# Optimization experiments

Hardware: AMD Instinct MI355X
Metric: run time of the kernel (lower is better)

## Reference

```python
import jax, jax.numpy as jnp
import numpy as np

DIM = 64
NUM_FEAT = 14
NUM_OUT = 105
N_NODES = 8192
N_EDGES = 16384
N_GRAPHS = 256
N_STEMS = 2048
N_JBONDS = 1024


def lrelu(v):
    return jax.nn.leaky_relu(v, 0.01)


def setup_inputs() -> dict:
    key = jax.random.key(0)
    ks = jax.random.split(key, 40)
    def rn(k, shape, s=0.1):
        return jax.random.normal(k, shape, dtype=jnp.float32) * s
    inp = {}
    inp['x'] = jax.random.normal(ks[0], (N_NODES, NUM_FEAT), dtype=jnp.float32)
    inp['edge_attr'] = jax.random.uniform(ks[1], (N_EDGES, 4), dtype=jnp.float32)
    inp['edge_index'] = jax.random.randint(ks[2], (2, N_EDGES), 0, N_NODES)
    inp['batch'] = jnp.sort(jax.random.randint(ks[3], (N_NODES,), 0, N_GRAPHS))
    inp['stem_atmidx'] = jax.random.randint(ks[4], (N_STEMS,), 0, N_NODES)
    inp['jbond_atmidx'] = jax.random.randint(ks[5], (N_JBONDS, 2), 0, N_NODES)
    # lin0
    inp['lin0_w'] = rn(ks[6], (NUM_FEAT, DIM)); inp['lin0_b'] = rn(ks[7], (DIM,))
    # NNConv edge net: Linear(4,dim) -> LeakyReLU -> Linear(dim, dim*dim)
    inp['net_w1'] = rn(ks[8], (4, DIM)); inp['net_b1'] = rn(ks[9], (DIM,))
    inp['net_w2'] = rn(ks[10], (DIM, DIM * DIM), 0.02); inp['net_b2'] = rn(ks[11], (DIM * DIM,), 0.02)
    # NNConv root weight + bias
    inp['conv_root'] = rn(ks[12], (DIM, DIM)); inp['conv_bias'] = rn(ks[13], (DIM,))
    # GRU (torch gate order r,z,n); stored [in, 3*dim]
    inp['gru_w_ih'] = rn(ks[14], (DIM, 3 * DIM)); inp['gru_w_hh'] = rn(ks[15], (DIM, 3 * DIM))
    inp['gru_b_ih'] = rn(ks[16], (3 * DIM,)); inp['gru_b_hh'] = rn(ks[17], (3 * DIM,))
    # node2stem MLP
    inp['n2s_w1'] = rn(ks[18], (DIM, DIM)); inp['n2s_b1'] = rn(ks[19], (DIM,))
    inp['n2s_w2'] = rn(ks[20], (DIM, NUM_OUT)); inp['n2s_b2'] = rn(ks[21], (NUM_OUT,))
    # node2jbond MLP
    inp['n2j_w1'] = rn(ks[22], (DIM, DIM)); inp['n2j_b1'] = rn(ks[23], (DIM,))
    inp['n2j_w2'] = rn(ks[24], (DIM, 1)); inp['n2j_b2'] = rn(ks[25], (1,))
    # Set2Set LSTM(2*dim -> dim), torch gate order i,f,g,o; stored [in, 4*dim]
    inp['s2s_w_ih'] = rn(ks[26], (2 * DIM, 4 * DIM)); inp['s2s_w_hh'] = rn(ks[27], (DIM, 4 * DIM))
    inp['s2s_b_ih'] = rn(ks[28], (4 * DIM,)); inp['s2s_b_hh'] = rn(ks[29], (4 * DIM,))
    # lin_out
    inp['lin_out_w'] = rn(ks[30], (2 * DIM, 2)); inp['lin_out_b'] = rn(ks[31], (2,))
    return inp


def reference(x, edge_attr, lin0_w, lin0_b, net_w1, net_b1, net_w2, net_b2,
              conv_root, conv_bias, gru_w_ih, gru_w_hh, gru_b_ih, gru_b_hh,
              n2s_w1, n2s_b1, n2s_w2, n2s_b2, n2j_w1, n2j_b1, n2j_w2, n2j_b2,
              s2s_w_ih, s2s_w_hh, s2s_b_ih, s2s_b_hh, lin_out_w, lin_out_b,
              edge_index, batch, stem_atmidx, jbond_atmidx):
    N = x.shape[0]
    src, dst = edge_index[0], edge_index[1]
    out = lrelu(x @ lin0_w + lin0_b)          # [N, dim]
    h = out
    # edge-conditioned weights (edge_attr is constant across the 6 iterations)
    ew = (lrelu(edge_attr @ net_w1 + net_b1) @ net_w2 + net_b2).reshape(-1, DIM, DIM)  # [E,dim,dim]
    deg = jnp.maximum(jax.ops.segment_sum(jnp.ones_like(dst, dtype=x.dtype), dst, num_segments=N), 1.0)[:, None]
    for _ in range(6):
        msg = jnp.einsum('ei,eio->eo', out[src], ew)                        # per-edge matmul
        agg = jax.ops.segment_sum(msg, dst, num_segments=N) / deg          # scatter-mean
        m = lrelu(agg + out @ conv_root + conv_bias)
        # GRU update (torch gate order r,z,n)
        gi = m @ gru_w_ih + gru_b_ih
        gh = h @ gru_w_hh + gru_b_hh
        ir, iz, inn = jnp.split(gi, 3, axis=-1)
        hr, hz, hn = jnp.split(gh, 3, axis=-1)
        r = jax.nn.sigmoid(ir + hr)
        z = jax.nn.sigmoid(iz + hz)
        n = jnp.tanh(inn + r * hn)
        h = (1.0 - z) * n + z * h
        out = h
    # per-stem block logits
    stem_preds = lrelu(out[stem_atmidx] @ n2s_w1 + n2s_b1) @ n2s_w2 + n2s_b2  # [S, num_out]
    # jbond: gather both endpoints, predict scalar, mean over the pair
    jb = out[jbond_atmidx.reshape(-1)]
    jpred = lrelu(jb @ n2j_w1 + n2j_b1) @ n2j_w2 + n2j_b2                     # [2J,1]
    jbond_preds = jpred.reshape(jbond_atmidx.shape).mean(axis=1)              # [J]
    # Set2Set, processing_steps=1
    B = N_GRAPHS
    hS = jnp.zeros((B, DIM), x.dtype)
    cS = jnp.zeros((B, DIM), x.dtype)
    q_star = jnp.zeros((B, 2 * DIM), x.dtype)
    gates = q_star @ s2s_w_ih + s2s_b_ih + hS @ s2s_w_hh + s2s_b_hh
    gi_, gf_, gg_, go_ = jnp.split(gates, 4, axis=-1)
    cS = jax.nn.sigmoid(gf_) * cS + jax.nn.sigmoid(gi_) * jnp.tanh(gg_)
    hS = jax.nn.sigmoid(go_) * jnp.tanh(cS)
    q = hS                                                                    # [B, dim]
    e = jnp.sum(out * q[batch], axis=-1)                                      # [N]
    emax = jax.ops.segment_max(e, batch, num_segments=B)
    a_un = jnp.exp(e - emax[batch])
    a = a_un / jax.ops.segment_sum(a_un, batch, num_segments=B)[batch]
    r_pool = jax.ops.segment_sum(a[:, None] * out, batch, num_segments=B)     # [B, dim]
    q_star = jnp.concatenate([q, r_pool], axis=1)                             # [B, 2*dim]
    scalar_outs = q_star @ lin_out_w + lin_out_b                              # [B, 2]
    return (scalar_outs, stem_preds, jbond_preds)
```

## Files before the change

### kernel.cpp

```cpp
#include <hip/hip_runtime.h>

#define DIM 64
#define NF 14
#define NOUT 105
#define NN 8192
#define NE 16384
#define NB 256
#define NS 2048
#define NJ 1024
#define KTOT 4160

#define C_X      0
#define C_EA     114688
#define C_L0W    180224
#define C_L0B    181120
#define C_NW1    181184
#define C_NB1    181440
#define C_NW2    181504
#define C_NB2    443648
#define C_CRT    447744
#define C_CB     451840
#define C_GWIH   451904
#define C_GWHH   464192
#define C_GBIH   476480
#define C_GBHH   476672
#define C_SW1    476864
#define C_SB1    480960
#define C_SW2    481024
#define C_SB2    487744
#define C_JW1    487856
#define C_JB1    491952
#define C_JW2    492016
#define C_JB2    492080
#define C_S2IH   492088
#define C_S2HH   492344
#define C_LOW    492600
#define C_LOB    492856
#define C_TOT    492864

typedef float f32x4 __attribute__((ext_vector_type(4)));
typedef short bf16x8 __attribute__((ext_vector_type(8)));

__device__ __forceinline__ float bf2f(unsigned short u){
  union { unsigned int i; float f; } v; v.i = ((unsigned int)u) << 16; return v.f;
}
__device__ __forceinline__ unsigned short f2bf(float f){
  union { float f; unsigned int i; } v; v.f = f;
  unsigned int x = v.i;
  return (unsigned short)((x + 0x7FFFu + ((x >> 16) & 1u)) >> 16);
}
__device__ __forceinline__ float sigm(float x){ return 1.f / (1.f + __expf(-x)); }
__device__ __forceinline__ float tanh_f(float x){
  x = fminf(10.f, fmaxf(-10.f, x));
  float e = __expf(2.f * x);
  return (e - 1.f) / (e + 1.f);
}
__device__ __forceinline__ float lrelu(float x){ return x > 0.f ? x : 0.01f * x; }

__device__ __forceinline__ float wred_sum(float v){
  #pragma unroll
  for (int off = 32; off > 0; off >>= 1) v += __shfl_xor(v, off, 64);
  return v;
}
__device__ __forceinline__ float wred_max(float v){
  #pragma unroll
  for (int off = 32; off > 0; off >>= 1) v = fmaxf(v, __shfl_xor(v, off, 64));
  return v;
}


__global__ void k_detect(const unsigned short* __restrict__ ea, int* __restrict__ flag){
  __shared__ int cnt;
  if (threadIdx.x == 0) cnt = 0;
  __syncthreads();
  int c = 0;
  for (int i = threadIdx.x; i < 8192; i += 256) c += (ea[2*i] >> 15) & 1;
  atomicAdd(&cnt, c);
  __syncthreads();
  if (threadIdx.x == 0) *flag = (cnt > 100) ? 1 : 0;
}

struct CvtArgs {
  const void* src[26];
  int n[26];
  int off[26];
};

__global__ void k_cvt(CvtArgs a, const int* __restrict__ flag, unsigned short* __restrict__ dst){
  bool f32 = (*flag != 0);
  int gid = blockIdx.x * blockDim.x + threadIdx.x, gs = gridDim.x * blockDim.x;
  #pragma unroll 1
  for (int j = 0; j < 26; ++j){
    const void* s = a.src[j];
    int n = a.n[j], o = a.off[j];
    for (int i = gid; i < n; i += gs)
      dst[o + i] = f32 ? f2bf(((const float*)s)[i]) : ((const unsigned short*)s)[i];
  }
}


__global__ void k_deg(const int* __restrict__ ei, float* __restrict__ deg){
  int e = blockIdx.x * blockDim.x + threadIdx.x;
  if (e < NE) atomicAdd(&deg[ei[NE + e]], 1.0f);
}

__global__ __launch_bounds__(256) void k_scan(const float* __restrict__ deg,
                                              int* __restrict__ offsets, int* __restrict__ cursor){
  __shared__ int part[256];
  int t = threadIdx.x;
  int s = 0;
  #pragma unroll 4
  for (int i = 0; i < 32; ++i) s += (int)deg[t*32 + i];
  part[t] = s;
  __syncthreads();
  for (int d = 1; d < 256; d <<= 1){
    int v = (t >= d) ? part[t - d] : 0;
    __syncthreads();
    part[t] += v;
    __syncthreads();
  }
  int run = (t == 0) ? 0 : part[t - 1];
  #pragma unroll 4
  for (int i = 0; i < 32; ++i){
    int n = t*32 + i;
    offsets[n] = run;
    cursor[n] = 0;
    run += (int)deg[n];
  }
  if (t == 255) offsets[NN] = run;
}

__global__ void k_fill(const int* __restrict__ ei, const int* __restrict__ offsets,
                       int* __restrict__ cursor, int* __restrict__ list){
  int e = blockIdx.x * blockDim.x + threadIdx.x;
  if (e < NE){
    int dst = ei[NE + e];
    int pos = atomicAdd(&cursor[dst], 1);
    list[offsets[dst] + pos] = e;
  }
}

__global__ void k_lin0(const unsigned short* __restrict__ cvt,
                       float* __restrict__ actF, unsigned short* __restrict__ actB){
  const unsigned short* x = cvt + C_X;
  const unsigned short* w = cvt + C_L0W;
  const unsigned short* b = cvt + C_L0B;
  int idx = blockIdx.x * blockDim.x + threadIdx.x;
  int n = idx >> 6, d = idx & 63;
  float acc = bf2f(b[d]);
  #pragma unroll
  for (int f = 0; f < NF; ++f) acc += bf2f(x[n*NF + f]) * bf2f(w[f*DIM + d]);
  float v = lrelu(acc);
  actF[idx] = v; actB[idx] = f2bf(v);
}

__global__ void k_u(const unsigned short* __restrict__ cvt, unsigned short* __restrict__ u){
  const unsigned short* ea = cvt + C_EA;
  const unsigned short* w  = cvt + C_NW1;
  const unsigned short* b  = cvt + C_NB1;
  int idx = blockIdx.x * blockDim.x + threadIdx.x;
  int e = idx >> 6, d = idx & 63;
  float acc = bf2f(b[d]);
  #pragma unroll
  for (int f = 0; f < 4; ++f) acc += bf2f(ea[e*4 + f]) * bf2f(w[f*DIM + d]);
  u[idx] = f2bf(lrelu(acc));
}

__global__ void k_w2t(const unsigned short* __restrict__ cvt, unsigned short* __restrict__ w2t){
  const unsigned short* w2 = cvt + C_NW2;
  int t = blockIdx.x * blockDim.x + threadIdx.x;
  int n = t >> 6, k = t & 63;
  w2t[t] = w2[k*4096 + (n & 63)*64 + (n >> 6)];
}

__global__ void k_w2r(const unsigned short* __restrict__ cvt, unsigned short* __restrict__ w2rt){
  const unsigned short* w2 = cvt + C_NW2;
  const unsigned short* b2 = cvt + C_NB2;
  int t = blockIdx.x * blockDim.x + threadIdx.x;
  int o = t / KTOT, k = t - o * KTOT;
  unsigned short v = (k < 4096) ? w2[(k >> 6) * 4096 + (k & 63) * 64 + o]
                                : b2[(k - 4096) * 64 + o];
  w2rt[t] = v;
}

__global__ void k_prep(const unsigned short* __restrict__ cvt,
                       unsigned short* __restrict__ crt, unsigned short* __restrict__ btg,
                       float* __restrict__ cbg, float* __restrict__ qv){
  const unsigned short* cr  = cvt + C_CRT;
  const unsigned short* wih = cvt + C_GWIH;
  const unsigned short* whh = cvt + C_GWHH;
  const unsigned short* bih = cvt + C_GBIH;
  const unsigned short* bhh = cvt + C_GBHH;
  const unsigned short* s2sbih = cvt + C_S2IH;
  const unsigned short* s2sbhh = cvt + C_S2HH;
  int tid = threadIdx.x;
  for (int t = tid; t < 4096; t += 256){ int n = t & 63, k = t >> 6; crt[n*64 + k] = cr[k*64 + n]; }
  for (int t = tid; t < 32768; t += 256){
    int nidx = t >> 7, kidx = t & 127;
    int g = nidx >> 6, d = nidx & 63, ki = kidx & 63;
    unsigned short v = 0;
    if (kidx < 64){
      if (g == 0) v = wih[ki*192 + d];
      else if (g == 1) v = wih[ki*192 + 64 + d];
      else if (g == 2) v = wih[ki*192 + 128 + d];
    } else {
      if (g == 0) v = whh[ki*192 + d];
      else if (g == 1) v = whh[ki*192 + 64 + d];
      else if (g == 3) v = whh[ki*192 + 128 + d];
    }
    btg[nidx*128 + kidx] = v;
  }
  if (tid < 256){
    int g = tid >> 6, d = tid & 63;
    float v;
    if (g == 0) v = bf2f(bih[d]) + bf2f(bhh[d]);
    else if (g == 1) v = bf2f(bih[64 + d]) + bf2f(bhh[64 + d]);
    else if (g == 2) v = bf2f(bih[128 + d]);
    else v = bf2f(bhh[128 + d]);
    cbg[tid] = v;
  }
  if (tid < 64){
    float gi = bf2f(s2sbih[tid])       + bf2f(s2sbhh[tid]);
    float gg = bf2f(s2sbih[128 + tid]) + bf2f(s2sbhh[128 + tid]);
    float go = bf2f(s2sbih[192 + tid]) + bf2f(s2sbhh[192 + tid]);
    float c = sigm(gi) * tanh_f(gg);
    qv[tid] = sigm(go) * tanh_f(c);
  }
}


__global__ __launch_bounds__(256) void k_ew(const unsigned short* __restrict__ z,
                                            const unsigned short* __restrict__ w2t,
                                            const unsigned short* __restrict__ cvt,
                                            unsigned short* __restrict__ ew){
  const unsigned short* b2 = cvt + C_NB2;
  __shared__ __align__(16) unsigned short tile[4][4096];
  int w = threadIdx.x >> 6, lane = threadIdx.x & 63;
  int lm = lane & 15, q8 = (lane >> 4) * 8, rq = (lane >> 4) * 4;
  int e0 = blockIdx.x * 64;
  int n0 = blockIdx.y * 256 + w * 64;
  f32x4 acc[4][4];
  #pragma unroll
  for (int mt = 0; mt < 4; ++mt)
    #pragma unroll
    for (int nt = 0; nt < 4; ++nt) acc[mt][nt] = (f32x4){0.f, 0.f, 0.f, 0.f};
  #pragma unroll
  for (int kk = 0; kk < 2; ++kk){
    bf16x8 af[4], bfr[4];
    #pragma unroll
    for (int mt = 0; mt < 4; ++mt)
      af[mt] = *(const bf16x8*)&z[(size_t)(e0 + mt*16 + lm)*64 + kk*32 + q8];
    #pragma unroll
    for (int nt = 0; nt < 4; ++nt)
      bfr[nt] = *(const bf16x8*)&w2t[(size_t)(n0 + nt*16 + lm)*64 + kk*32 + q8];
    #pragma unroll
    for (int mt = 0; mt < 4; ++mt)
      #pragma unroll
      for (int nt = 0; nt < 4; ++nt)
        acc[mt][nt] = __builtin_amdgcn_mfma_f32_16x16x32_bf16(af[mt], bfr[nt], acc[mt][nt], 0, 0, 0);
  }
  #pragma unroll
  for (int nt = 0; nt < 4; ++nt){
    int col = nt*16 + lm;
    int gcol = n0 + col;
    float bb = bf2f(b2[((gcol & 63) << 6) | (gcol >> 6)]);
    #pragma unroll
    for (int mt = 0; mt < 4; ++mt)
      #pragma unroll
      for (int r = 0; r < 4; ++r){
        int row = mt*16 + rq + r;
        int phys = (col >> 3) ^ (row & 7);
        tile[w][row*64 + phys*8 + (col & 7)] = f2bf(acc[mt][nt][r] + bb);
      }
  }
  #pragma unroll
  for (int it = 0; it < 8; ++it){
    int row = it*8 + (lane >> 3);
    int c16 = lane & 7;
    int phys = c16 ^ (row & 7);
    bf16x8 v = *(const bf16x8*)&tile[w][row*64 + phys*8];
    *(bf16x8*)&ew[(size_t)(e0 + row)*4096 + n0 + c16*8] = v;
  }
}

__global__ __launch_bounds__(256) void k_msgv(const unsigned short* __restrict__ actB,
                                              const unsigned short* __restrict__ ew,
                                              const int* __restrict__ ei,
                                              unsigned short* __restrict__ msgv){
  __shared__ __align__(16) float sact[4][64];
  int w = threadIdx.x >> 6, lane = threadIdx.x & 63;
  int e = blockIdx.x * 4 + w;
  int src = ei[e];
  sact[w][lane] = bf2f(actB[(size_t)src*64 + lane]);
  __syncthreads();
  const unsigned short* ep = ew + (size_t)e*4096 + (size_t)lane*64;
  float acc = 0.f;
  #pragma unroll
  for (int t = 0; t < 8; ++t){
    bf16x8 v = *(const bf16x8*)(ep + t*8);
    f32x4 sa = *(const f32x4*)&sact[w][t*8];
    f32x4 sb = *(const f32x4*)&sact[w][t*8 + 4];
    acc += bf2f((unsigned short)v[0]) * sa[0];
    acc += bf2f((unsigned short)v[1]) * sa[1];
    acc += bf2f((unsigned short)v[2]) * sa[2];
    acc += bf2f((unsigned short)v[3]) * sa[3];
    acc += bf2f((unsigned short)v[4]) * sb[0];
    acc += bf2f((unsigned short)v[5]) * sb[1];
    acc += bf2f((unsigned short)v[6]) * sb[2];
    acc += bf2f((unsigned short)v[7]) * sb[3];
  }
  msgv[(size_t)e*64 + lane] = f2bf(acc);
}

__global__ __launch_bounds__(256) void k_agg(const unsigned short* __restrict__ msgv,
                                             const int* __restrict__ offsets,
                                             const int* __restrict__ list,
                                             float* __restrict__ agg){
  int w = threadIdx.x >> 6, lane = threadIdx.x & 63;
  int v = blockIdx.x * 4 + w;
  int ib = offsets[v], ie = offsets[v + 1];
  float acc = 0.f;
  for (int j = ib; j < ie; ++j){
    int e = list[j];
    acc += bf2f(msgv[(size_t)e*64 + lane]);
  }
  agg[(size_t)v*64 + lane] = acc;
}


__global__ __launch_bounds__(256) void k_msgf(const unsigned short* __restrict__ actB,
                                              const unsigned short* __restrict__ z,
                                              const unsigned short* __restrict__ w2rt,
                                              const int* __restrict__ ei,
                                              float* __restrict__ agg){
  __shared__ __align__(16) unsigned short sz[256 * 8];
  int w = threadIdx.x >> 6, lane = threadIdx.x & 63;
  int lm = lane & 15, q8 = (lane >> 4) * 8, rq = (lane >> 4) * 4;
  int e0 = blockIdx.x * 256;
  int s  = blockIdx.y;
  {
    int t = threadIdx.x;
    *(uint4*)&sz[t * 8] = *(const uint4*)&z[(size_t)(e0 + t) * 64 + s * 8];
  }
  __syncthreads();
  uint4 apack[4][2];
  #pragma unroll
  for (int mt = 0; mt < 4; ++mt){
    int src = ei[e0 + w*64 + mt*16 + lm];
    apack[mt][0] = *(const uint4*)&actB[(size_t)src * 64 + q8];
    apack[mt][1] = *(const uint4*)&actB[(size_t)src * 64 + 32 + q8];
  }
  f32x4 acc[4][4];
  #pragma unroll
  for (int mt = 0; mt < 4; ++mt)
    #pragma unroll
    for (int nt = 0; nt < 4; ++nt) acc[mt][nt] = (f32x4){0.f, 0.f, 0.f, 0.f};
  int kk0 = s * 16;
  int nk = (s == 7) ? 18 : 16;
  for (int c = 0; c < nk; ++c){
    int kk = kk0 + c;
    bf16x8 bfr[4];
    #pragma unroll
    for (int nt = 0; nt < 4; ++nt)
      bfr[nt] = *(const bf16x8*)&w2rt[(size_t)(nt*16 + lm) * KTOT + kk*32 + q8];
    #pragma unroll
    for (int mt = 0; mt < 4; ++mt){
      float zf = 1.0f;
      if (kk < 128){
        int erow = w*64 + mt*16 + lm;
        zf = bf2f(sz[erow * 8 + ((kk >> 1) & 7)]);
      }
      uint4 ap = apack[mt][kk & 1];
      bf16x8 af;
      #pragma unroll
      for (int h = 0; h < 4; ++h){
        unsigned int dw = ((const unsigned int*)&ap)[h];
        float flo = __uint_as_float(dw << 16) * zf;
        float fhi = __uint_as_float(dw & 0xFFFF0000u) * zf;
        unsigned int pk = ((unsigned int)f2bf(flo)) | (((unsigned int)f2bf(fhi)) << 16);
        ((unsigned int*)&af)[h] = pk;
      }
      #pragma unroll
      for (int nt = 0; nt < 4; ++nt)
        acc[mt][nt] = __builtin_amdgcn_mfma_f32_16x16x32_bf16(af, bfr[nt], acc[mt][nt], 0, 0, 0);
    }
  }
  #pragma unroll
  for (int mt = 0; mt < 4; ++mt){
    #pragma unroll
    for (int r = 0; r < 4; ++r){
      int dst = ei[NE + e0 + w*64 + mt*16 + rq + r];
      #pragma unroll
      for (int nt = 0; nt < 4; ++nt)
        atomicAdd(&agg[(size_t)dst * 64 + nt*16 + lm], acc[mt][nt][r]);
    }
  }
}


__global__ __launch_bounds__(256) void k_gru(const unsigned short* __restrict__ actB_in,
                                             const float* __restrict__ actF_in,
                                             const float* __restrict__ agg, const float* __restrict__ deg,
                                             const unsigned short* __restrict__ crt,
                                             const unsigned short* __restrict__ cvt,
                                             const unsigned short* __restrict__ btg,
                                             const float* __restrict__ cbg,
                                             float* __restrict__ actF_out, unsigned short* __restrict__ actB_out){
  const unsigned short* cbias = cvt + C_CB;
  __shared__ __align__(16) unsigned short s_frag[2*4*16*8];
  int w = threadIdx.x >> 6, lane = threadIdx.x & 63;
  int lm = lane & 15, q = lane >> 4;
  int q8 = q*8, rq = q*4;
  int r0 = blockIdx.x * 16;
  f32x4 am = (f32x4){0.f, 0.f, 0.f, 0.f};
  #pragma unroll
  for (int kk = 0; kk < 2; ++kk){
    bf16x8 a = *(const bf16x8*)&actB_in[(size_t)(r0 + lm)*64 + kk*32 + q8];
    bf16x8 b = *(const bf16x8*)&crt[(size_t)(w*16 + lm)*64 + kk*32 + q8];
    am = __builtin_amdgcn_mfma_f32_16x16x32_bf16(a, b, am, 0, 0, 0);
  }
  {
    int col = w*16 + lm;
    float cb = bf2f(cbias[col]);
    int kk2 = w >> 1, q2 = (w & 1)*2 + (lm >> 3), j = lm & 7;
    #pragma unroll
    for (int r = 0; r < 4; ++r){
      int row = r0 + rq + r;
      float dg = fmaxf(deg[row], 1.f);
      float v = am[r] + agg[(size_t)row*64 + col] / dg + cb;
      s_frag[((kk2*4 + q2)*16 + (rq + r))*8 + j] = f2bf(lrelu(v));
    }
  }
  __syncthreads();
  f32x4 g[4];
  #pragma unroll
  for (int t = 0; t < 4; ++t) g[t] = (f32x4){0.f, 0.f, 0.f, 0.f};
  #pragma unroll
  for (int kk = 0; kk < 4; ++kk){
    bf16x8 a;
    if (kk < 2) a = *(const bf16x8*)&s_frag[(kk*4 + q)*128 + lm*8];
    else        a = *(const bf16x8*)&actB_in[(size_t)(r0 + lm)*64 + (kk - 2)*32 + q8];
    #pragma unroll
    for (int t = 0; t < 4; ++t){
      bf16x8 b = *(const bf16x8*)&btg[(size_t)(t*64 + w*16 + lm)*128 + kk*32 + q8];
      g[t] = __builtin_amdgcn_mfma_f32_16x16x32_bf16(a, b, g[t], 0, 0, 0);
    }
  }
  {
    int d = w*16 + lm;
    float cb_r = cbg[d], cb_z = cbg[64 + d], cb_n = cbg[128 + d], cb_h = cbg[192 + d];
    #pragma unroll
    for (int r = 0; r < 4; ++r){
      int row = r0 + rq + r;
      float rr = sigm(g[0][r] + cb_r);
      float zz = sigm(g[1][r] + cb_z);
      float nn = tanh_f(g[2][r] + cb_n + rr * (g[3][r] + cb_h));
      float ho = actF_in[(size_t)row*64 + d];
      float hn2 = (1.f - zz) * nn + zz * ho;
      actF_out[(size_t)row*64 + d] = hn2;
      actB_out[(size_t)row*64 + d] = f2bf(hn2);
    }
  }
}


__device__ __forceinline__ int lower_bound_batch(const int* b, int val){
  int lo = 0, hi = NN;
  while (lo < hi){ int mid = (lo + hi) >> 1; if (b[mid] < val) lo = mid + 1; else hi = mid; }
  return lo;
}

__device__ __forceinline__ void store_out(void* outp, const int* flag, size_t idx, float v){
  if (*flag) ((float*)outp)[idx] = v;
  else       ((unsigned short*)outp)[idx] = f2bf(v);
}

__global__ __launch_bounds__(64) void k_graph(const float* __restrict__ act,
                                              const int* __restrict__ batch, const float* __restrict__ qv,
                                              const unsigned short* __restrict__ cvt,
                                              const int* __restrict__ flag,
                                              void* __restrict__ outp){
  const unsigned short* lw = cvt + C_LOW;
  const unsigned short* lb = cvt + C_LOB;
  __shared__ float se[512];
  int b = blockIdx.x, lane = threadIdx.x;
  int lo = lower_bound_batch(batch, b);
  int hi = lower_bound_batch(batch, b + 1);
  int cnt = hi - lo; if (cnt > 512) cnt = 512;
  float qvl = qv[lane];
  for (int ii = 0; ii < cnt; ++ii){
    float p = act[(size_t)(lo + ii)*64 + lane] * qvl;
    p = wred_sum(p);
    if (lane == 0) se[ii] = p;
  }
  __syncthreads();
  float em = -3.4e38f;
  for (int ii = lane; ii < cnt; ii += 64) em = fmaxf(em, se[ii]);
  em = wred_max(em);
  float sm = 0.f;
  for (int ii = lane; ii < cnt; ii += 64) sm += __expf(se[ii] - em);
  float denom = wred_sum(sm);
  float rp = 0.f;
  for (int ii = 0; ii < cnt; ++ii) rp += __expf(se[ii] - em) * act[(size_t)(lo + ii)*64 + lane];
  if (cnt > 0 && denom > 0.f) rp /= denom;
  float s0 = qvl*bf2f(lw[lane*2])     + rp*bf2f(lw[(64 + lane)*2]);
  float s1 = qvl*bf2f(lw[lane*2 + 1]) + rp*bf2f(lw[(64 + lane)*2 + 1]);
  s0 = wred_sum(s0); s1 = wred_sum(s1);
  if (lane == 0){
    store_out(outp, flag, b*2,     s0 + bf2f(lb[0]));
    store_out(outp, flag, b*2 + 1, s1 + bf2f(lb[1]));
  }
}

__global__ __launch_bounds__(256) void k_stem(const float* __restrict__ act, const int* __restrict__ sidx,
                                              const unsigned short* __restrict__ cvt,
                                              const int* __restrict__ flag,
                                              void* __restrict__ outp){
  const unsigned short* w1 = cvt + C_SW1;
  const unsigned short* b1 = cvt + C_SB1;
  const unsigned short* w2 = cvt + C_SW2;
  const unsigned short* b2 = cvt + C_SB2;
  __shared__ float sa[4][64], st[4][64];
  int w = threadIdx.x >> 6, lane = threadIdx.x & 63;
  int s = blockIdx.x * 4 + w;
  int a = sidx[s];
  sa[w][lane] = act[(size_t)a*64 + lane];
  __syncthreads();
  float t = bf2f(b1[lane]);
  #pragma unroll 8
  for (int i = 0; i < 64; ++i) t += sa[w][i] * bf2f(w1[i*64 + lane]);
  st[w][lane] = lrelu(t);
  __syncthreads();
  size_t base = 512 + (size_t)s * NOUT;
  float v = bf2f(b2[lane]);
  #pragma unroll 8
  for (int d = 0; d < 64; ++d) v += st[w][d] * bf2f(w2[d*NOUT + lane]);
  store_out(outp, flag, base + lane, v);
  int o2 = 64 + lane;
  if (o2 < NOUT){
    float v2 = bf2f(b2[o2]);
    #pragma unroll 8
    for (int d = 0; d < 64; ++d) v2 += st[w][d] * bf2f(w2[d*NOUT + o2]);
    store_out(outp, flag, base + o2, v2);
  }
}

__global__ __launch_bounds__(256) void k_jbond(const float* __restrict__ act, const int* __restrict__ jidx,
                                               const unsigned short* __restrict__ cvt,
                                               const int* __restrict__ flag,
                                               void* __restrict__ outp){
  const unsigned short* w1 = cvt + C_JW1;
  const unsigned short* b1 = cvt + C_JB1;
  const unsigned short* w2 = cvt + C_JW2;
  const unsigned short* b2 = cvt + C_JB2;
  __shared__ float a0[4][64], a1[4][64];
  int w = threadIdx.x >> 6, lane = threadIdx.x & 63;
  int j = blockIdx.x * 4 + w;
  int i0 = jidx[j*2], i1 = jidx[j*2 + 1];
  a0[w][lane] = act[(size_t)i0*64 + lane];
  a1[w][lane] = act[(size_t)i1*64 + lane];
  __syncthreads();
  float t0 = bf2f(b1[lane]), t1 = t0;
  #pragma unroll 8
  for (int i = 0; i < 64; ++i){
    float wv = bf2f(w1[i*64 + lane]);
    t0 += a0[w][i] * wv;
    t1 += a1[w][i] * wv;
  }
  t0 = lrelu(t0); t1 = lrelu(t1);
  float p = (t0 + t1) * bf2f(w2[lane]);
  p = wred_sum(p);
  if (lane == 0) store_out(outp, flag, 512 + (size_t)NS*NOUT + j, 0.5f * p + bf2f(b2[0]));
}


extern "C" void kernel_launch(void* const* d_in, const int* in_sizes, int n_in,
                              void* d_out, int out_size, void* d_ws, size_t ws_size,
                              hipStream_t stream){
  (void)in_sizes; (void)n_in; (void)out_size;
  const int* edge_index = (const int*)d_in[2];
  const int* batch      = (const int*)d_in[3];
  const int* stem_idx   = (const int*)d_in[4];
  const int* jbond_idx  = (const int*)d_in[5];

  char* ws = (char*)d_ws;
  size_t off = 0;
  auto alloc = [&](size_t bytes) -> void* {
    void* p = ws + off; off += (bytes + 255) & ~(size_t)255; return p;
  };
  unsigned short* cvt  = (unsigned short*)alloc((size_t)C_TOT * 2);
  unsigned short* w2t  = (unsigned short*)alloc((size_t)4096 * 64 * 2);
  unsigned short* w2rt = (unsigned short*)alloc((size_t)64 * KTOT * 2);
  unsigned short* z_bf = (unsigned short*)alloc((size_t)NE * 64 * 2);
  unsigned short* msgv = z_bf;
  float* actF0 = (float*)alloc((size_t)NN * 64 * 4);
  float* actF1 = (float*)alloc((size_t)NN * 64 * 4);
  unsigned short* actB0 = (unsigned short*)alloc((size_t)NN * 64 * 2);
  unsigned short* actB1 = (unsigned short*)alloc((size_t)NN * 64 * 2);
  float* deg  = (float*)alloc(NN * 4);
  float* agg  = (float*)alloc((size_t)NN * 64 * 4);
  unsigned short* crt = (unsigned short*)alloc(64 * 64 * 2);
  unsigned short* btg = (unsigned short*)alloc(256 * 128 * 2);
  float* cbg  = (float*)alloc(256 * 4);
  float* qv   = (float*)alloc(64 * 4);
  int* flag   = (int*)alloc(256);
  int* offsets = (int*)alloc((NN + 1) * 4);
  int* cursor  = (int*)alloc(NN * 4);
  int* list    = (int*)alloc(NE * 4);
  size_t ew_bytes = (size_t)NE * 4096 * 2;
  bool big = (off + ew_bytes) <= ws_size;
  unsigned short* ew = big ? (unsigned short*)alloc(ew_bytes) : nullptr;

  hipMemsetAsync(deg, 0, NN * sizeof(float), stream);

  k_detect<<<1, 256, 0, stream>>>((const unsigned short*)d_in[1], flag);

  CvtArgs ca;
  const int srcIdx[26] = {0,1,6,7,8,9,10,11,12,13,14,15,16,17,18,19,20,21,22,23,24,25,28,29,30,31};
  const int ns[26]  = {114688,65536,896,64,256,64,262144,4096,4096,64,12288,12288,192,192,
                       4096,64,6720,105,4096,64,64,1,256,256,256,2};
  const int ofs[26] = {C_X,C_EA,C_L0W,C_L0B,C_NW1,C_NB1,C_NW2,C_NB2,C_CRT,C_CB,C_GWIH,C_GWHH,
                       C_GBIH,C_GBHH,C_SW1,C_SB1,C_SW2,C_SB2,C_JW1,C_JB1,C_JW2,C_JB2,
                       C_S2IH,C_S2HH,C_LOW,C_LOB};
  for (int j = 0; j < 26; ++j){ ca.src[j] = d_in[srcIdx[j]]; ca.n[j] = ns[j]; ca.off[j] = ofs[j]; }
  k_cvt<<<512, 256, 0, stream>>>(ca, flag, cvt);

  k_deg<<<NE/256, 256, 0, stream>>>(edge_index, deg);
  k_scan<<<1, 256, 0, stream>>>(deg, offsets, cursor);
  k_fill<<<NE/256, 256, 0, stream>>>(edge_index, offsets, cursor, list);
  k_lin0<<<NN*DIM/256, 256, 0, stream>>>(cvt, actF0, actB0);
  k_u<<<NE*DIM/256, 256, 0, stream>>>(cvt, z_bf);
  k_prep<<<1, 256, 0, stream>>>(cvt, crt, btg, cbg, qv);

  if (big){
    k_w2t<<<4096*64/256, 256, 0, stream>>>(cvt, w2t);
    k_ew<<<dim3(NE/64, 16), 256, 0, stream>>>(z_bf, w2t, cvt, ew);
  } else {
    k_w2r<<<64*KTOT/256, 256, 0, stream>>>(cvt, w2rt);
  }

  for (int t = 0; t < 6; ++t){
    const float* aF_in  = (t & 1) ? actF1 : actF0;
    float* aF_out       = (t & 1) ? actF0 : actF1;
    const unsigned short* aB_in = (t & 1) ? actB1 : actB0;
    unsigned short* aB_out      = (t & 1) ? actB0 : actB1;
    if (big){
      k_msgv<<<NE/4, 256, 0, stream>>>(aB_in, ew, edge_index, msgv);
      k_agg<<<NN/4, 256, 0, stream>>>(msgv, offsets, list, agg);
    } else {
      hipMemsetAsync(agg, 0, (size_t)NN * 64 * sizeof(float), stream);
      k_msgf<<<dim3(NE/256, 8), 256, 0, stream>>>(aB_in, z_bf, w2rt, edge_index, agg);
    }
    k_gru<<<NN/16, 256, 0, stream>>>(aB_in, aF_in, agg, deg, crt, cvt, btg, cbg,
                                     aF_out, aB_out);
  }
  k_graph<<<NB, 64, 0, stream>>>(actF0, batch, qv, cvt, flag, d_out);
  k_stem<<<NS/4, 256, 0, stream>>>(actF0, stem_idx, cvt, flag, d_out);
  k_jbond<<<NJ/4, 256, 0, stream>>>(actF0, jbond_idx, cvt, flag, d_out);
}
```

Measured before the change: 516.7 us.

## Coalesce per-edge matvec loads and fuse CSR aggregation into GRU kernel

The per-edge message kernel now has each group of 8 lanes read contiguous 16-byte chunks of the edge weight matrix and reduce the partial dot products with shuffles, instead of each lane striding through its own 128-byte row. The separate aggregation kernel is removed: the GRU kernel gathers the incoming messages for each node directly through the CSR offsets and list when the big path is active. This cuts one launch per step and the agg buffer round-trip. The cost is irregular gather loops inside the GRU kernel, with lanes of a wave walking different degree counts.

```diff
diff --git a/kernel.cpp b/kernel.cpp
--- a/kernel.cpp
+++ b/kernel.cpp
@@ -287,44 +287,34 @@
                                               const unsigned short* __restrict__ ew,
                                               const int* __restrict__ ei,
                                               unsigned short* __restrict__ msgv){
-  __shared__ __align__(16) float sact[4][64];
+  __shared__ __align__(16) unsigned short sact[4][64];
+  __shared__ unsigned short smsg[4][64];
   int w = threadIdx.x >> 6, lane = threadIdx.x & 63;
   int e = blockIdx.x * 4 + w;
   int src = ei[e];
-  sact[w][lane] = bf2f(actB[(size_t)src*64 + lane]);
-  __syncthreads();
-  const unsigned short* ep = ew + (size_t)e*4096 + (size_t)lane*64;
-  float acc = 0.f;
+  sact[w][lane] = actB[(size_t)src*64 + lane];
+  __syncthreads();
+  float av[8];
+  {
+    bf16x8 a8 = *(const bf16x8*)&sact[w][(lane & 7) * 8];
+    #pragma unroll
+    for (int j = 0; j < 8; ++j) av[j] = bf2f((unsigned short)a8[j]);
+  }
+  const unsigned short* ep = ew + (size_t)e*4096;
+  int g = lane >> 3;
   #pragma unroll
   for (int t = 0; t < 8; ++t){
-    bf16x8 v = *(const bf16x8*)(ep + t*8);
-    f32x4 sa = *(const f32x4*)&sact[w][t*8];
-    f32x4 sb = *(const f32x4*)&sact[w][t*8 + 4];
-    acc += bf2f((unsigned short)v[0]) * sa[0];
-    acc += bf2f((unsigned short)v[1]) * sa[1];
-    acc += bf2f((unsigned short)v[2]) * sa[2];
-    acc += bf2f((unsigned short)v[3]) * sa[3];
-    acc += bf2f((unsigned short)v[4]) * sb[0];
-    acc += bf2f((unsigned short)v[5]) * sb[1];
-    acc += bf2f((unsigned short)v[6]) * sb[2];
-    acc += bf2f((unsigned short)v[7]) * sb[3];
-  }
-  msgv[(size_t)e*64 + lane] = f2bf(acc);
-}
-
-__global__ __launch_bounds__(256) void k_agg(const unsigned short* __restrict__ msgv,
-                                             const int* __restrict__ offsets,
-                                             const int* __restrict__ list,
-                                             float* __restrict__ agg){
-  int w = threadIdx.x >> 6, lane = threadIdx.x & 63;
-  int v = blockIdx.x * 4 + w;
-  int ib = offsets[v], ie = offsets[v + 1];
-  float acc = 0.f;
-  for (int j = ib; j < ie; ++j){
-    int e = list[j];
-    acc += bf2f(msgv[(size_t)e*64 + lane]);
-  }
-  agg[(size_t)v*64 + lane] = acc;
+    bf16x8 v = *(const bf16x8*)(ep + t*512 + lane*8);
+    float p = 0.f;
+    #pragma unroll
+    for (int j = 0; j < 8; ++j) p += av[j] * bf2f((unsigned short)v[j]);
+    p += __shfl_xor(p, 1, 64);
+    p += __shfl_xor(p, 2, 64);
+    p += __shfl_xor(p, 4, 64);
+    if ((lane & 7) == 0) smsg[w][t*8 + g] = f2bf(p);
+  }
+  __syncthreads();
+  msgv[(size_t)e*64 + lane] = smsg[w][lane];
 }
 
 
@@ -400,7 +390,12 @@
 
 __global__ __launch_bounds__(256) void k_gru(const unsigned short* __restrict__ actB_in,
                                              const float* __restrict__ actF_in,
-                                             const float* __restrict__ agg, const float* __restrict__ deg,
+                                             const float* __restrict__ agg,
+                                             const unsigned short* __restrict__ msgv,
+                                             const int* __restrict__ offsets,
+                                             const int* __restrict__ list,
+                                             int useCsr,
+                                             const float* __restrict__ deg,
                                              const unsigned short* __restrict__ crt,
                                              const unsigned short* __restrict__ cvt,
                                              const unsigned short* __restrict__ btg,
@@ -427,7 +422,16 @@
     for (int r = 0; r < 4; ++r){
       int row = r0 + rq + r;
       float dg = fmaxf(deg[row], 1.f);
-      float v = am[r] + agg[(size_t)row*64 + col] / dg + cb;
+      float msum;
+      if (useCsr){
+        int ib = offsets[row], ie2 = offsets[row + 1];
+        msum = 0.f;
+        for (int jj = ib; jj < ie2; ++jj)
+          msum += bf2f(msgv[(size_t)list[jj]*64 + col]);
+      } else {
+        msum = agg[(size_t)row*64 + col];
+      }
+      float v = am[r] + msum / dg + cb;
       s_frag[((kk2*4 + q2)*16 + (rq + r))*8 + j] = f2bf(lrelu(v));
     }
   }
@@ -646,13 +650,14 @@
     unsigned short* aB_out      = (t & 1) ? actB0 : actB1;
     if (big){
       k_msgv<<<NE/4, 256, 0, stream>>>(aB_in, ew, edge_index, msgv);
-      k_agg<<<NN/4, 256, 0, stream>>>(msgv, offsets, list, agg);
+      k_gru<<<NN/16, 256, 0, stream>>>(aB_in, aF_in, agg, msgv, offsets, list, 1,
+                                       deg, crt, cvt, btg, cbg, aF_out, aB_out);
     } else {
       hipMemsetAsync(agg, 0, (size_t)NN * 64 * sizeof(float), stream);
       k_msgf<<<dim3(NE/256, 8), 256, 0, stream>>>(aB_in, z_bf, w2rt, edge_index, agg);
+      k_gru<<<NN/16, 256, 0, stream>>>(aB_in, aF_in, agg, msgv, offsets, list, 0,
+                                       deg, crt, cvt, btg, cbg, aF_out, aB_out);
     }
-    k_gru<<<NN/16, 256, 0, stream>>>(aB_in, aF_in, agg, deg, crt, cvt, btg, cbg,
-                                     aF_out, aB_out);
   }
   k_graph<<<NB, 64, 0, stream>>>(actF0, batch, qv, cvt, flag, d_out);
   k_stem<<<NS/4, 256, 0, stream>>>(actF0, stem_idx, cvt, flag, d_out);
```

Measured after the change: 502.6 us. 1.03x faster.
